# Performance work log

Measured on AMD Instinct MI355X. Metric: run time of the kernel, lower is better.

The kernel has to match this reference:

```python
import jax, jax.numpy as jnp
import numpy as np

B, D, K, NC, F = 2048, 256, 256, 64, 512
EPS = 1e-3           # transport_eps
TAU_MIN = 0.01
TAU_DENOM_MIN = 1e-3


def setup_inputs() -> dict:
    key = jax.random.key(0)
    ks = jax.random.split(key, 8)
    # latents strictly inside the Poincare ball (norm ~0.5 for D=256)
    z = 0.03 * jax.random.normal(ks[0], (B, D), jnp.float32)
    features = jax.random.normal(ks[1], (B, F), jnp.float32)
    # SpectralLinear params (treated as plain linear layers in the reference)
    W_qz = 0.02 * jax.random.normal(ks[2], (K, D), jnp.float32)
    b_qz = jnp.zeros((K,), jnp.float32)
    W_qf = 0.02 * jax.random.normal(ks[3], (K, F), jnp.float32)
    b_qf = jnp.zeros((K,), jnp.float32)
    # full tensorization gamma: [K, D, D]
    q_gamma = 0.02 * jax.random.normal(ks[4], (K, D, D), jnp.float32)
    chart_queries = 0.02 * jax.random.normal(ks[5], (NC, K), jnp.float32)
    return {
        "z": z, "features": features,
        "W_qz": W_qz, "b_qz": b_qz, "W_qf": W_qf, "b_qf": b_qf,
        "q_gamma": q_gamma, "chart_queries": chart_queries,
    }


def reference(z, features, W_qz, b_qz, W_qf, b_qf, q_gamma, chart_queries):
    # centers = chart_queries[:, :latent_dim] (chart_tokens=None path); D == K here
    centers = chart_queries[:, :D]                      # [NC, D]

    # ---- hyperbolic (Poincare ball) distance scores ----
    r2 = jnp.sum(z * z, axis=-1)                        # [B]
    c_sq = jnp.sum(centers * centers, axis=-1)          # [NC]
    diff = z[:, None, :] - centers[None, :, :]          # [B, NC, D]
    dist_sq = jnp.sum(diff * diff, axis=-1)             # [B, NC]
    denom = (1.0 - r2[:, None]) * (1.0 - c_sq[None, :])
    arg = 1.0 + 2.0 * dist_sq / (denom + EPS)
    dist = jnp.arccosh(jnp.maximum(arg, 1.0 + EPS))

    # metric-aware temperature tau(z)
    tau = jnp.maximum(
        jnp.sqrt(jnp.float32(K)) * jnp.maximum(1.0 - r2, TAU_DENOM_MIN) * 0.5,
        TAU_MIN,
    )                                                   # [B]
    scores = -dist / tau[:, None]                       # [B, NC]

    # ---- feature-based refinement (q_feat_proj branch) ----
    q = z @ W_qz.T + b_qz + features @ W_qf.T + b_qf    # [B, K]
    # gamma term: einsum('bij,kij->bk', z outer z, q_gamma) without [B,D,D]
    gz = jnp.einsum('bj,kij->bki', z, q_gamma)          # [B, K, D]
    q = q + jnp.einsum('bki,bi->bk', gz, z)             # [B, K]

    # transported queries: base_queries / lambda(z); (Q/lam) . q == (q @ Q.T)/lam
    r2c = jnp.minimum(r2, 1.0 - EPS)
    lam = 2.0 / (1.0 - r2c + EPS)                       # [B]
    feature_scores = (q @ chart_queries.T) / lam[:, None]  # [B, NC]

    scores = scores + 0.1 * feature_scores / tau[:, None]

    router_weights = jax.nn.softmax(scores, axis=-1)    # [B, NC]
    K_chart = jnp.argmax(router_weights, axis=-1)       # [B]
    return router_weights, K_chart
```

## Files before the change

kernel.cpp:

```cpp
#include <hip/hip_runtime.h>
#include <hip/hip_bf16.h>
#include <hip/hip_fp16.h>


#define B_SZ 2048
#define D_SZ 256
#define K_SZ 256
#define NC_SZ 64
#define F_SZ 512
#define P_SZ 65536

typedef float  floatx4  __attribute__((ext_vector_type(4)));
typedef float  floatx16 __attribute__((ext_vector_type(16)));
typedef _Float16 h8 __attribute__((ext_vector_type(8)));
typedef __fp16  fp16x2 __attribute__((ext_vector_type(2)));
union H8U4 { uint4 u; h8 h; };

#define WS_BEFF  49152
#define WS_CSQ   49216
#define WS_Q2    65664
#define WS_MH    196736
#define WS_WALL  2293888
#define WS_PART  2351232

__device__ __forceinline__ unsigned pkrtz_u(float a, float b) {
    fp16x2 r = __builtin_amdgcn_cvt_pkrtz(a, b);
    return __builtin_bit_cast(unsigned, r);
}
__device__ __forceinline__ _Float16 h16rtz(float x) {
    fp16x2 r = __builtin_amdgcn_cvt_pkrtz(x, x);
    return (_Float16)r[0];
}
__device__ __forceinline__ unsigned packh2(_Float16 a, _Float16 b) {
    union { _Float16 h[2]; unsigned u; } r; r.h[0] = a; r.h[1] = b; return r.u;
}

__device__ __forceinline__ void gload16(const void* g, void* l) {
    __builtin_amdgcn_global_load_lds(
        (const __attribute__((address_space(1))) unsigned*)g,
        (__attribute__((address_space(3))) unsigned*)l, 16, 0, 0);
}

__global__ __launch_bounds__(256) void prep_kernel(
        const float* __restrict__ Wqz, const float* __restrict__ bqz,
        const float* __restrict__ Wqf, const float* __restrict__ bqf,
        const float* __restrict__ cq,  float* __restrict__ ws) {
    const int tid = threadIdx.x;
    const int w = tid >> 6, c = tid & 63;
    const int bid = blockIdx.x;
    char* wall = (char*)(ws + WS_WALL);

    if (bid >= 193) {
        _Float16* cqh = (_Float16*)(ws + WS_Q2);
        const int idx = (bid - 193)*256 + tid;
        const floatx4* sp = (const floatx4*)(cq + idx*8);
        floatx4 a = sp[0], b = sp[1];
        uint4 u = { pkrtz_u(a[0],a[1]), pkrtz_u(a[2],a[3]),
                    pkrtz_u(b[0],b[1]), pkrtz_u(b[2],b[3]) };
        *(uint4*)(cqh + idx*8) = u;
        return;
    }

    __shared__ float cqL[64*257];
    #pragma unroll
    for (int s = 0; s < 16; ++s) {
        const int e4 = s*256 + tid;
        const int row = e4 >> 6, col = (e4 & 63)*4;
        floatx4 v = *(const floatx4*)(cq + e4*4);
        #pragma unroll
        for (int u = 0; u < 4; ++u) cqL[row*257 + col + u] = v[u];
    }
    __syncthreads();

    if (bid < 64) {
        const int i = bid*4 + w;
        float a0 = 0.f, a1 = 0.f, a2 = 0.f, a3 = 0.f;
        #pragma unroll 8
        for (int k = 0; k < K_SZ; k += 4) {
            a0 = fmaf(cqL[c*257 + k    ], Wqz[(k    )*D_SZ + i], a0);
            a1 = fmaf(cqL[c*257 + k + 1], Wqz[(k + 1)*D_SZ + i], a1);
            a2 = fmaf(cqL[c*257 + k + 2], Wqz[(k + 2)*D_SZ + i], a2);
            a3 = fmaf(cqL[c*257 + k + 3], Wqz[(k + 3)*D_SZ + i], a3);
        }
        const float acc = (a0 + a1) + (a2 + a3);
        const int boff = c*512 + ((((i >> 3) & 31) ^ (c & 31)) << 4) + (i & 7)*2;
        *(_Float16*)(wall + 0*32768 + boff) = (_Float16)acc;
        const float v = cqL[c*257 + i];
        const _Float16 vh = (_Float16)v;
        *(_Float16*)(wall + 5*32768 + boff) = vh;
        *(_Float16*)(wall + 6*32768 + boff) =
            h16rtz((v - (float)vh) * 1024.f);
    } else if (bid < 192) {
        const int j = (bid - 64)*4 + w;
        float a0 = 0.f, a1 = 0.f, a2 = 0.f, a3 = 0.f;
        #pragma unroll 8
        for (int k = 0; k < K_SZ; k += 4) {
            a0 = fmaf(cqL[c*257 + k    ], Wqf[(k    )*F_SZ + j], a0);
            a1 = fmaf(cqL[c*257 + k + 1], Wqf[(k + 1)*F_SZ + j], a1);
            a2 = fmaf(cqL[c*257 + k + 2], Wqf[(k + 2)*F_SZ + j], a2);
            a3 = fmaf(cqL[c*257 + k + 3], Wqf[(k + 3)*F_SZ + j], a3);
        }
        const float acc = (a0 + a1) + (a2 + a3);
        const int row = j & 255;
        const int sbase = (j < 256) ? 1 : 3;
        const int boff = c*512 + ((((row >> 3) & 31) ^ (c & 31)) << 4) + (row & 7)*2;
        const _Float16 ah = (_Float16)acc;
        *(_Float16*)(wall + (size_t)sbase*32768 + boff) = ah;
        *(_Float16*)(wall + (size_t)(sbase + 1)*32768 + boff) =
            h16rtz((acc - (float)ah) * 1024.f);
    } else {
        if (w == 0) {
            float acc = 0.f;
            for (int k = 0; k < K_SZ; ++k)
                acc = fmaf(cqL[c*257 + k], bqz[k] + bqf[k], acc);
            ws[WS_BEFF + c] = acc;
        } else if (w == 1) {
            float acc = 0.f;
            for (int i = 0; i < D_SZ; ++i) {
                const float v = cqL[c*257 + i];
                acc = fmaf(v, v, acc);
            }
            ws[WS_CSQ + c] = acc;
        }
    }
}

__global__ __launch_bounds__(256, 4) void mc_kernel(
        const float* __restrict__ gamma, const _Float16* __restrict__ cqh,
        _Float16* __restrict__ mh) {
    const int tid = threadIdx.x;
    const int w = tid >> 6, lane = tid & 63;
    const int ln = lane & 31, half = lane >> 5;
    const int mt = w >> 1, ns = w & 1;
    const int p0 = blockIdx.x * 64;
    const int iseg = p0 >> 8, j0 = p0 & 255;
    const int rot = blockIdx.x & 15;

    floatx16 acc;
    #pragma unroll
    for (int r = 0; r < 16; ++r) acc[r] = 0.f;

    const int arow = mt*32 + ln;
    const float* __restrict__ gbase = gamma + (size_t)(half*8)*P_SZ + p0 + ns*32 + ln;

    #pragma unroll 2
    for (int t = 0; t < 16; ++t) {
        const int kc = (t + rot) & 15;
        float g[8];
        #pragma unroll
        for (int kk = 0; kk < 8; ++kk)
            g[kk] = gbase[(size_t)(kc*16 + kk)*P_SZ];
        H8U4 a; a.u = *(const uint4*)(cqh + arow*256 + kc*16 + half*8);
        H8U4 b;
        b.u.x = pkrtz_u(g[0], g[1]);
        b.u.y = pkrtz_u(g[2], g[3]);
        b.u.z = pkrtz_u(g[4], g[5]);
        b.u.w = pkrtz_u(g[6], g[7]);
        acc = __builtin_amdgcn_mfma_f32_32x32x16_f16(a.h, b.h, acc, 0, 0, 0);
    }
    #pragma unroll
    for (int r = 0; r < 16; ++r) {
        const int cc = mt*32 + (r&3) + 8*(r>>2) + 4*half;
        const int j  = j0 + ns*32 + ln;
        const int jc = j >> 3, off = j & 7;
        mh[(size_t)cc*P_SZ + iseg*256 + ((jc ^ (cc&31))*8 + off)] = (_Float16)acc[r];
    }
}

__global__ __launch_bounds__(256) void qf_kernel(
        const float* __restrict__ z, const _Float16* __restrict__ mh,
        float* __restrict__ part) {
    __shared__ __align__(16) char bt[2][64 * 512];
    const int tid = threadIdx.x;
    const int w = tid >> 6, lane = tid & 63;
    const int ln = lane & 31, half = lane >> 5;
    const int bid = blockIdx.x;
    const int xcd = bid & 7;
    const int y   = bid >> 3;
    const int ig  = xcd*4 + (y & 3);
    const int b0  = (y >> 2) * 128;
    const int bb = b0 + w*32 + ln;

    #define STAGE(i, sel)                                                     \
        _Pragma("unroll")                                                     \
        for (int s = 0; s < 8; ++s) {                                         \
            const int e = s*256 + tid;                                        \
            gload16((const char*)mh +                                         \
                    ((size_t)(e >> 5)*P_SZ + (size_t)(i)*256)*2 + (e & 31)*16,\
                    bt[sel] + e*16);                                          \
        }

    STAGE(ig*8, 0);

    uint4 zjh[16];
    #pragma unroll
    for (int ch = 0; ch < 16; ++ch) {
        const floatx4* zp = (const floatx4*)(z + bb*D_SZ + ch*16 + half*8);
        floatx4 a = zp[0], b = zp[1];
        zjh[ch].x = pkrtz_u(a[0], a[1]);
        zjh[ch].y = pkrtz_u(a[2], a[3]);
        zjh[ch].z = pkrtz_u(b[0], b[1]);
        zjh[ch].w = pkrtz_u(b[2], b[3]);
    }
    float ziv[8];
    {
        const floatx4* zp = (const floatx4*)(z + bb*D_SZ + ig*8);
        floatx4 a = zp[0], b = zp[1];
        #pragma unroll
        for (int t = 0; t < 4; ++t) { ziv[t] = a[t]; ziv[4+t] = b[t]; }
    }

    floatx16 acc0, acc1;
    #pragma unroll
    for (int r = 0; r < 16; ++r) { acc0[r] = 0.f; acc1[r] = 0.f; }

    for (int il = 0; il < 8; ++il) {
        __syncthreads();
        if (il < 7) { STAGE(ig*8 + il + 1, (il + 1) & 1); }

        const float zi = ziv[il];
        const unsigned zu = pkrtz_u(zi, zi);
        H8U4 zb; zb.u.x = zu; zb.u.y = zu; zb.u.z = zu; zb.u.w = zu;
        const char* btc = bt[il & 1];
        __builtin_amdgcn_s_setprio(1);
        #pragma unroll
        for (int ch = 0; ch < 16; ++ch) {
            H8U4 aj; aj.u = zjh[ch];
            h8 af = aj.h * zb.h;
            const int pc = ((ch*2 + half) ^ ln) * 16;
            H8U4 f0, f1;
            f0.u = *(const uint4*)(btc + ln*512 + pc);
            f1.u = *(const uint4*)(btc + (32 + ln)*512 + pc);
            acc0 = __builtin_amdgcn_mfma_f32_32x32x16_f16(af, f0.h, acc0, 0, 0, 0);
            acc1 = __builtin_amdgcn_mfma_f32_32x32x16_f16(af, f1.h, acc1, 0, 0, 0);
        }
        __builtin_amdgcn_s_setprio(0);
    }
    #undef STAGE

    float* __restrict__ qp = part + (size_t)ig * (B_SZ * NC_SZ);
    #pragma unroll
    for (int r = 0; r < 16; ++r) {
        const int row  = (r&3) + 8*(r>>2) + 4*half;
        const int brow = b0 + w*32 + row;
        qp[brow*NC_SZ + ln]      = acc0[r];
        qp[brow*NC_SZ + 32 + ln] = acc1[r];
    }
}

__global__ __launch_bounds__(256) void lin2_kernel(
        const float* __restrict__ z, const float* __restrict__ feat,
        const float* __restrict__ wall_f, float* __restrict__ part,
        float* __restrict__ dot) {
    __shared__ __align__(16) char bt[2][64 * 512];
    const char* wall = (const char*)wall_f;
    const int tid = threadIdx.x;
    const int w = tid >> 6, lane = tid & 63;
    const int ln = lane & 31, half = lane >> 5;
    const int b0 = blockIdx.x * 128;
    const int s  = blockIdx.y;
    const int bb = b0 + w*32 + ln;
    const int s_hi = (s == 0) ? 0 : (s == 1) ? 1 : (s == 2) ? 3 : 5;

    #pragma unroll
    for (int e0 = 0; e0 < 8; ++e0) {
        const int e = e0*256 + tid;
        gload16(wall + s_hi*32768 + e*16, bt[0] + e*16);
    }
    if (s > 0) {
        #pragma unroll
        for (int e0 = 0; e0 < 8; ++e0) {
            const int e = e0*256 + tid;
            gload16(wall + (s_hi + 1)*32768 + e*16, bt[1] + e*16);
        }
    }
    const float* __restrict__ arow =
        (s == 0 || s == 3) ? z + bb*D_SZ : feat + bb*F_SZ + (s == 2 ? 256 : 0);
    __syncthreads();

    floatx16 hh0, hh1, lh0, lh1, hl0, hl1;
    #pragma unroll
    for (int r = 0; r < 16; ++r) {
        hh0[r] = 0.f; hh1[r] = 0.f; lh0[r] = 0.f;
        lh1[r] = 0.f; hl0[r] = 0.f; hl1[r] = 0.f;
    }

    #pragma unroll
    for (int ch = 0; ch < 16; ++ch) {
        const floatx4* ap = (const floatx4*)(arow + ch*16 + half*8);
        floatx4 a4 = ap[0], b4 = ap[1];
        float vv[8];
        #pragma unroll
        for (int t = 0; t < 4; ++t) { vv[t] = a4[t]; vv[4+t] = b4[t]; }
        _Float16 hc[8];
        #pragma unroll
        for (int j = 0; j < 8; ++j) hc[j] = (_Float16)vv[j];
        H8U4 ah;
        ah.u.x = packh2(hc[0], hc[1]); ah.u.y = packh2(hc[2], hc[3]);
        ah.u.z = packh2(hc[4], hc[5]); ah.u.w = packh2(hc[6], hc[7]);

        const int pc = ((ch*2 + half) ^ ln) * 16;
        H8U4 f0, f1;
        f0.u = *(const uint4*)(bt[0] + ln*512 + pc);
        f1.u = *(const uint4*)(bt[0] + (32 + ln)*512 + pc);
        hh0 = __builtin_amdgcn_mfma_f32_32x32x16_f16(ah.h, f0.h, hh0, 0, 0, 0);
        hh1 = __builtin_amdgcn_mfma_f32_32x32x16_f16(ah.h, f1.h, hh1, 0, 0, 0);

        if (s > 0) {
            float l[8];
            #pragma unroll
            for (int j = 0; j < 8; ++j) l[j] = (vv[j] - (float)hc[j]) * 1024.f;
            H8U4 al;
            al.u.x = pkrtz_u(l[0], l[1]); al.u.y = pkrtz_u(l[2], l[3]);
            al.u.z = pkrtz_u(l[4], l[5]); al.u.w = pkrtz_u(l[6], l[7]);
            H8U4 g0, g1;
            g0.u = *(const uint4*)(bt[1] + ln*512 + pc);
            g1.u = *(const uint4*)(bt[1] + (32 + ln)*512 + pc);
            lh0 = __builtin_amdgcn_mfma_f32_32x32x16_f16(al.h, f0.h, lh0, 0, 0, 0);
            lh1 = __builtin_amdgcn_mfma_f32_32x32x16_f16(al.h, f1.h, lh1, 0, 0, 0);
            hl0 = __builtin_amdgcn_mfma_f32_32x32x16_f16(ah.h, g0.h, hl0, 0, 0, 0);
            hl1 = __builtin_amdgcn_mfma_f32_32x32x16_f16(ah.h, g1.h, hl1, 0, 0, 0);
        }
    }

    const float is = 1.0f / 1024.0f;
    float* __restrict__ qp = part + (size_t)(32 + s) * (B_SZ * NC_SZ);
    #pragma unroll
    for (int r = 0; r < 16; ++r) {
        const int row  = (r&3) + 8*(r>>2) + 4*half;
        const int brow = b0 + w*32 + row;
        float v0 = hh0[r], v1 = hh1[r];
        if (s > 0) { v0 += (lh0[r] + hl0[r])*is; v1 += (lh1[r] + hl1[r])*is; }
        if (s < 3) {
            qp[brow*NC_SZ + ln]      = v0;
            qp[brow*NC_SZ + 32 + ln] = v1;
        } else {
            dot[brow*NC_SZ + ln]      = v0;
            dot[brow*NC_SZ + 32 + ln] = v1;
        }
    }
}

__global__ __launch_bounds__(256) void final_kernel(
        const float* __restrict__ z, const float* __restrict__ ws,
        const float* __restrict__ dot, float* __restrict__ out) {
    const int w = threadIdx.x >> 6, c = threadIdx.x & 63;
    const int b = blockIdx.x*4 + w;

    const floatx4 zv = *(const floatx4*)(z + b*D_SZ + c*4);
    float r2 = zv[0]*zv[0] + zv[1]*zv[1] + zv[2]*zv[2] + zv[3]*zv[3];
    #pragma unroll
    for (int off = 32; off > 0; off >>= 1)
        r2 += __shfl_xor(r2, off, 64);

    const float* __restrict__ part = ws + WS_PART;
    float Q = ws[WS_BEFF + c];
    #pragma unroll
    for (int p = 0; p < 35; ++p)
        Q += part[(size_t)p * (B_SZ*NC_SZ) + b*NC_SZ + c];

    const float csq = ws[WS_CSQ + c];
    const float dsq = fmaf(-2.f, dot[b*64 + c], r2) + csq;

    const double r2d = (double)r2, csqd = (double)csq, dsqd = (double)dsq;
    const double denom = (1.0 - r2d) * (1.0 - csqd);
    double arg = 1.0 + 2.0 * dsqd / (denom + 0.001);
    if (arg < 1.001) arg = 1.001;
    const double dist = acosh(arg);
    double tmp = 1.0 - r2d; if (tmp < 0.001) tmp = 0.001;
    double tau = 8.0 * tmp;
    if (tau < 0.01) tau = 0.01;
    double r2c = r2d; if (r2c > 0.999) r2c = 0.999;
    const double lam = 2.0 / (1.0 - r2c + 0.001);
    const double score = -dist / tau + 0.1 * ((double)Q / lam) / tau;

    double m = score;
    #pragma unroll
    for (int off = 32; off > 0; off >>= 1) {
        double o = __shfl_xor(m, off, 64);
        m = fmax(m, o);
    }
    const double e = exp(score - m);
    double s = e;
    #pragma unroll
    for (int off = 32; off > 0; off >>= 1) s += __shfl_xor(s, off, 64);
    out[b*NC_SZ + c] = (float)(e / s);

    double bsc = score; int bix = c;
    #pragma unroll
    for (int off = 32; off > 0; off >>= 1) {
        double osc = __shfl_xor(bsc, off, 64);
        int    oix = __shfl_xor(bix, off, 64);
        if (osc > bsc || (osc == bsc && oix < bix)) { bsc = osc; bix = oix; }
    }
    if (c == 0) out[B_SZ*NC_SZ + b] = (float)bix;
}

extern "C" void kernel_launch(void* const* d_in, const int* in_sizes, int n_in,
                              void* d_out, int out_size, void* d_ws, size_t ws_size,
                              hipStream_t stream) {
    const float* z    = (const float*)d_in[0];
    const float* feat = (const float*)d_in[1];
    const float* Wqz  = (const float*)d_in[2];
    const float* bqz  = (const float*)d_in[3];
    const float* Wqf  = (const float*)d_in[4];
    const float* bqf  = (const float*)d_in[5];
    const float* gamma= (const float*)d_in[6];
    const float* cq   = (const float*)d_in[7];
    float* out = (float*)d_out;
    float* ws  = (float*)d_ws;
    _Float16* cqh = (_Float16*)(ws + WS_Q2);
    _Float16* mh  = (_Float16*)(ws + WS_MH);
    float*    dot = ws + WS_MH;

    prep_kernel<<<201, 256, 0, stream>>>(Wqz, bqz, Wqf, bqf, cq, ws);
    mc_kernel<<<1024, 256, 0, stream>>>(gamma, cqh, mh);
    qf_kernel<<<512, 256, 0, stream>>>(z, mh, ws + WS_PART);
    lin2_kernel<<<dim3(16, 4), 256, 0, stream>>>(z, feat, ws + WS_WALL,
                                                 ws + WS_PART, dot);
    final_kernel<<<512, 256, 0, stream>>>(z, ws, dot, out);
}
```

Measured before the change: 179.2 us.

## Merge prep and gamma-contraction kernels, merge qf and lin2 kernels, halve LDS tiles

Cuts the pipeline from five launches to three. The prep work and the gamma-by-chart-query MFMA contraction now share one grid, with the query-to-fp16 conversion done inline so the separate cqh buffer is gone. The gamma-quadratic partials and the split-fp16 linear projections also run in one grid. LDS tiles are halved (16 KB double buffers, cqL processed in two 128-wide halves) to raise occupancy, at the cost of more stage/sync iterations. The dot output moves to its own workspace region so it no longer aliases mh, which the fused kernel still reads.

```diff
diff --git a/kernel.cpp b/kernel.cpp
--- a/kernel.cpp
+++ b/kernel.cpp
@@ -18,10 +18,10 @@
 
 #define WS_BEFF  49152
 #define WS_CSQ   49216
-#define WS_Q2    65664
 #define WS_MH    196736
 #define WS_WALL  2293888
 #define WS_PART  2351232
+#define WS_DOT   6938752
 
 __device__ __forceinline__ unsigned pkrtz_u(float a, float b) {
     fp16x2 r = __builtin_amdgcn_cvt_pkrtz(a, b);
@@ -41,65 +41,128 @@
         (__attribute__((address_space(3))) unsigned*)l, 16, 0, 0);
 }
 
-__global__ __launch_bounds__(256) void prep_kernel(
-        const float* __restrict__ Wqz, const float* __restrict__ bqz,
-        const float* __restrict__ Wqf, const float* __restrict__ bqf,
-        const float* __restrict__ cq,  float* __restrict__ ws) {
+__global__ __launch_bounds__(256, 4) void mid_kernel(
+        const float* __restrict__ gamma, const float* __restrict__ cq,
+        const float* __restrict__ Wqz,  const float* __restrict__ bqz,
+        const float* __restrict__ Wqf,  const float* __restrict__ bqf,
+        float* __restrict__ ws, _Float16* __restrict__ mh) {
+    __shared__ float cqL[64*129];
     const int tid = threadIdx.x;
+    const int bid = blockIdx.x;
+
+    if (bid < 1024) {
+        const int w = tid >> 6, lane = tid & 63;
+        const int ln = lane & 31, half = lane >> 5;
+        const int mt = w >> 1, ns = w & 1;
+        const int p0 = bid * 64;
+        const int iseg = p0 >> 8, j0 = p0 & 255;
+        const int rot = bid & 15;
+
+        floatx16 acc;
+        #pragma unroll
+        for (int r = 0; r < 16; ++r) acc[r] = 0.f;
+
+        const int arow = mt*32 + ln;
+        const float* __restrict__ cqrow = cq + arow*256;
+        const float* __restrict__ gbase =
+            gamma + (size_t)(half*8)*P_SZ + p0 + ns*32 + ln;
+
+        #pragma unroll 2
+        for (int t = 0; t < 16; ++t) {
+            const int kc = (t + rot) & 15;
+            float g[8];
+            #pragma unroll
+            for (int kk = 0; kk < 8; ++kk)
+                g[kk] = gbase[(size_t)(kc*16 + kk)*P_SZ];
+            const floatx4* cp = (const floatx4*)(cqrow + kc*16 + half*8);
+            floatx4 ca = cp[0], cb = cp[1];
+            H8U4 a;
+            a.u.x = pkrtz_u(ca[0], ca[1]); a.u.y = pkrtz_u(ca[2], ca[3]);
+            a.u.z = pkrtz_u(cb[0], cb[1]); a.u.w = pkrtz_u(cb[2], cb[3]);
+            H8U4 b;
+            b.u.x = pkrtz_u(g[0], g[1]);
+            b.u.y = pkrtz_u(g[2], g[3]);
+            b.u.z = pkrtz_u(g[4], g[5]);
+            b.u.w = pkrtz_u(g[6], g[7]);
+            acc = __builtin_amdgcn_mfma_f32_32x32x16_f16(a.h, b.h, acc, 0, 0, 0);
+        }
+        #pragma unroll
+        for (int r = 0; r < 16; ++r) {
+            const int cc = mt*32 + (r&3) + 8*(r>>2) + 4*half;
+            const int j  = j0 + ns*32 + ln;
+            const int jc = j >> 3, off = j & 7;
+            mh[(size_t)cc*P_SZ + iseg*256 + ((jc ^ (cc&31))*8 + off)] =
+                (_Float16)acc[r];
+        }
+        return;
+    }
+
+    const int pbid = bid - 1024;
     const int w = tid >> 6, c = tid & 63;
-    const int bid = blockIdx.x;
     char* wall = (char*)(ws + WS_WALL);
 
-    if (bid >= 193) {
-        _Float16* cqh = (_Float16*)(ws + WS_Q2);
-        const int idx = (bid - 193)*256 + tid;
-        const floatx4* sp = (const floatx4*)(cq + idx*8);
-        floatx4 a = sp[0], b = sp[1];
-        uint4 u = { pkrtz_u(a[0],a[1]), pkrtz_u(a[2],a[3]),
-                    pkrtz_u(b[0],b[1]), pkrtz_u(b[2],b[3]) };
-        *(uint4*)(cqh + idx*8) = u;
-        return;
-    }
-
-    __shared__ float cqL[64*257];
-    #pragma unroll
-    for (int s = 0; s < 16; ++s) {
-        const int e4 = s*256 + tid;
-        const int row = e4 >> 6, col = (e4 & 63)*4;
-        floatx4 v = *(const floatx4*)(cq + e4*4);
-        #pragma unroll
-        for (int u = 0; u < 4; ++u) cqL[row*257 + col + u] = v[u];
-    }
-    __syncthreads();
-
-    if (bid < 64) {
-        const int i = bid*4 + w;
-        float a0 = 0.f, a1 = 0.f, a2 = 0.f, a3 = 0.f;
-        #pragma unroll 8
-        for (int k = 0; k < K_SZ; k += 4) {
-            a0 = fmaf(cqL[c*257 + k    ], Wqz[(k    )*D_SZ + i], a0);
-            a1 = fmaf(cqL[c*257 + k + 1], Wqz[(k + 1)*D_SZ + i], a1);
-            a2 = fmaf(cqL[c*257 + k + 2], Wqz[(k + 2)*D_SZ + i], a2);
-            a3 = fmaf(cqL[c*257 + k + 3], Wqz[(k + 3)*D_SZ + i], a3);
-        }
-        const float acc = (a0 + a1) + (a2 + a3);
+    float a0 = 0.f, a1 = 0.f, a2 = 0.f, a3 = 0.f;
+    float bacc = 0.f, cacc = 0.f, cqv = 0.f;
+    const int i_or_j = (pbid < 64) ? pbid*4 + w :
+                       (pbid < 192) ? (pbid - 64)*4 + w : 0;
+
+    for (int h = 0; h < 2; ++h) {
+        #pragma unroll
+        for (int s8 = 0; s8 < 8; ++s8) {
+            const int e4 = s8*256 + tid;
+            const int row = e4 >> 5, col4 = (e4 & 31)*4;
+            floatx4 v = *(const floatx4*)(cq + row*256 + h*128 + col4);
+            #pragma unroll
+            for (int u = 0; u < 4; ++u) cqL[row*129 + col4 + u] = v[u];
+        }
+        __syncthreads();
+
+        if (pbid < 64) {
+            const int i = i_or_j;
+            #pragma unroll 8
+            for (int kk = 0; kk < 128; kk += 4) {
+                const int k = h*128 + kk;
+                a0 = fmaf(cqL[c*129 + kk    ], Wqz[(k    )*D_SZ + i], a0);
+                a1 = fmaf(cqL[c*129 + kk + 1], Wqz[(k + 1)*D_SZ + i], a1);
+                a2 = fmaf(cqL[c*129 + kk + 2], Wqz[(k + 2)*D_SZ + i], a2);
+                a3 = fmaf(cqL[c*129 + kk + 3], Wqz[(k + 3)*D_SZ + i], a3);
+            }
+            if ((i >> 7) == h) cqv = cqL[c*129 + (i & 127)];
+        } else if (pbid < 192) {
+            const int j = i_or_j;
+            #pragma unroll 8
+            for (int kk = 0; kk < 128; kk += 4) {
+                const int k = h*128 + kk;
+                a0 = fmaf(cqL[c*129 + kk    ], Wqf[(k    )*F_SZ + j], a0);
+                a1 = fmaf(cqL[c*129 + kk + 1], Wqf[(k + 1)*F_SZ + j], a1);
+                a2 = fmaf(cqL[c*129 + kk + 2], Wqf[(k + 2)*F_SZ + j], a2);
+                a3 = fmaf(cqL[c*129 + kk + 3], Wqf[(k + 3)*F_SZ + j], a3);
+            }
+        } else {
+            if (w == 0) {
+                for (int kk = 0; kk < 128; ++kk) {
+                    const int k = h*128 + kk;
+                    bacc = fmaf(cqL[c*129 + kk], bqz[k] + bqf[k], bacc);
+                }
+            } else if (w == 1) {
+                for (int ii = 0; ii < 128; ++ii) {
+                    const float v = cqL[c*129 + ii];
+                    cacc = fmaf(v, v, cacc);
+                }
+            }
+        }
+        __syncthreads();
+    }
+
+    if (pbid < 64) {
+        const int i = i_or_j;
         const int boff = c*512 + ((((i >> 3) & 31) ^ (c & 31)) << 4) + (i & 7)*2;
-        *(_Float16*)(wall + 0*32768 + boff) = (_Float16)acc;
-        const float v = cqL[c*257 + i];
-        const _Float16 vh = (_Float16)v;
+        *(_Float16*)(wall + 0*32768 + boff) = (_Float16)((a0 + a1) + (a2 + a3));
+        const _Float16 vh = (_Float16)cqv;
         *(_Float16*)(wall + 5*32768 + boff) = vh;
-        *(_Float16*)(wall + 6*32768 + boff) =
-            h16rtz((v - (float)vh) * 1024.f);
-    } else if (bid < 192) {
-        const int j = (bid - 64)*4 + w;
-        float a0 = 0.f, a1 = 0.f, a2 = 0.f, a3 = 0.f;
-        #pragma unroll 8
-        for (int k = 0; k < K_SZ; k += 4) {
-            a0 = fmaf(cqL[c*257 + k    ], Wqf[(k    )*F_SZ + j], a0);
-            a1 = fmaf(cqL[c*257 + k + 1], Wqf[(k + 1)*F_SZ + j], a1);
-            a2 = fmaf(cqL[c*257 + k + 2], Wqf[(k + 2)*F_SZ + j], a2);
-            a3 = fmaf(cqL[c*257 + k + 3], Wqf[(k + 3)*F_SZ + j], a3);
-        }
+        *(_Float16*)(wall + 6*32768 + boff) = h16rtz((cqv - (float)vh) * 1024.f);
+    } else if (pbid < 192) {
+        const int j = i_or_j;
         const float acc = (a0 + a1) + (a2 + a3);
         const int row = j & 255;
         const int sbase = (j < 256) ? 1 : 3;
@@ -109,174 +172,119 @@
         *(_Float16*)(wall + (size_t)(sbase + 1)*32768 + boff) =
             h16rtz((acc - (float)ah) * 1024.f);
     } else {
-        if (w == 0) {
-            float acc = 0.f;
-            for (int k = 0; k < K_SZ; ++k)
-                acc = fmaf(cqL[c*257 + k], bqz[k] + bqf[k], acc);
-            ws[WS_BEFF + c] = acc;
-        } else if (w == 1) {
-            float acc = 0.f;
-            for (int i = 0; i < D_SZ; ++i) {
-                const float v = cqL[c*257 + i];
-                acc = fmaf(v, v, acc);
-            }
-            ws[WS_CSQ + c] = acc;
-        }
-    }
-}
-
-__global__ __launch_bounds__(256, 4) void mc_kernel(
-        const float* __restrict__ gamma, const _Float16* __restrict__ cqh,
-        _Float16* __restrict__ mh) {
+        if (w == 0) ws[WS_BEFF + c] = bacc;
+        else if (w == 1) ws[WS_CSQ + c] = cacc;
+    }
+}
+
+__global__ __launch_bounds__(256, 3) void qflin_kernel(
+        const float* __restrict__ z, const float* __restrict__ feat,
+        const _Float16* __restrict__ mh, const float* __restrict__ wall_f,
+        float* __restrict__ part, float* __restrict__ dot) {
+    __shared__ __align__(16) char bt[2][16384];
     const int tid = threadIdx.x;
     const int w = tid >> 6, lane = tid & 63;
     const int ln = lane & 31, half = lane >> 5;
-    const int mt = w >> 1, ns = w & 1;
-    const int p0 = blockIdx.x * 64;
-    const int iseg = p0 >> 8, j0 = p0 & 255;
-    const int rot = blockIdx.x & 15;
-
-    floatx16 acc;
-    #pragma unroll
-    for (int r = 0; r < 16; ++r) acc[r] = 0.f;
-
-    const int arow = mt*32 + ln;
-    const float* __restrict__ gbase = gamma + (size_t)(half*8)*P_SZ + p0 + ns*32 + ln;
-
-    #pragma unroll 2
-    for (int t = 0; t < 16; ++t) {
-        const int kc = (t + rot) & 15;
-        float g[8];
-        #pragma unroll
-        for (int kk = 0; kk < 8; ++kk)
-            g[kk] = gbase[(size_t)(kc*16 + kk)*P_SZ];
-        H8U4 a; a.u = *(const uint4*)(cqh + arow*256 + kc*16 + half*8);
-        H8U4 b;
-        b.u.x = pkrtz_u(g[0], g[1]);
-        b.u.y = pkrtz_u(g[2], g[3]);
-        b.u.z = pkrtz_u(g[4], g[5]);
-        b.u.w = pkrtz_u(g[6], g[7]);
-        acc = __builtin_amdgcn_mfma_f32_32x32x16_f16(a.h, b.h, acc, 0, 0, 0);
-    }
-    #pragma unroll
-    for (int r = 0; r < 16; ++r) {
-        const int cc = mt*32 + (r&3) + 8*(r>>2) + 4*half;
-        const int j  = j0 + ns*32 + ln;
-        const int jc = j >> 3, off = j & 7;
-        mh[(size_t)cc*P_SZ + iseg*256 + ((jc ^ (cc&31))*8 + off)] = (_Float16)acc[r];
-    }
-}
-
-__global__ __launch_bounds__(256) void qf_kernel(
-        const float* __restrict__ z, const _Float16* __restrict__ mh,
-        float* __restrict__ part) {
-    __shared__ __align__(16) char bt[2][64 * 512];
-    const int tid = threadIdx.x;
-    const int w = tid >> 6, lane = tid & 63;
-    const int ln = lane & 31, half = lane >> 5;
-    const int bid = blockIdx.x;
-    const int xcd = bid & 7;
-    const int y   = bid >> 3;
-    const int ig  = xcd*4 + (y & 3);
-    const int b0  = (y >> 2) * 128;
-    const int bb = b0 + w*32 + ln;
-
-    #define STAGE(i, sel)                                                     \
-        _Pragma("unroll")                                                     \
-        for (int s = 0; s < 8; ++s) {                                         \
-            const int e = s*256 + tid;                                        \
-            gload16((const char*)mh +                                         \
-                    ((size_t)(e >> 5)*P_SZ + (size_t)(i)*256)*2 + (e & 31)*16,\
-                    bt[sel] + e*16);                                          \
-        }
-
-    STAGE(ig*8, 0);
-
-    uint4 zjh[16];
-    #pragma unroll
-    for (int ch = 0; ch < 16; ++ch) {
-        const floatx4* zp = (const floatx4*)(z + bb*D_SZ + ch*16 + half*8);
-        floatx4 a = zp[0], b = zp[1];
-        zjh[ch].x = pkrtz_u(a[0], a[1]);
-        zjh[ch].y = pkrtz_u(a[2], a[3]);
-        zjh[ch].z = pkrtz_u(b[0], b[1]);
-        zjh[ch].w = pkrtz_u(b[2], b[3]);
-    }
-    float ziv[8];
-    {
-        const floatx4* zp = (const floatx4*)(z + bb*D_SZ + ig*8);
-        floatx4 a = zp[0], b = zp[1];
-        #pragma unroll
-        for (int t = 0; t < 4; ++t) { ziv[t] = a[t]; ziv[4+t] = b[t]; }
-    }
-
-    floatx16 acc0, acc1;
-    #pragma unroll
-    for (int r = 0; r < 16; ++r) { acc0[r] = 0.f; acc1[r] = 0.f; }
-
-    for (int il = 0; il < 8; ++il) {
-        __syncthreads();
-        if (il < 7) { STAGE(ig*8 + il + 1, (il + 1) & 1); }
-
-        const float zi = ziv[il];
-        const unsigned zu = pkrtz_u(zi, zi);
-        H8U4 zb; zb.u.x = zu; zb.u.y = zu; zb.u.z = zu; zb.u.w = zu;
-        const char* btc = bt[il & 1];
-        __builtin_amdgcn_s_setprio(1);
+
+    if (blockIdx.x >= 64) {
+        const int bid = blockIdx.x - 64;
+        const int xcd = bid & 7;
+        const int y   = bid >> 3;
+        const int ig  = xcd*4 + (y & 3);
+        const int b0  = (y >> 2) * 128;
+        const int bb  = b0 + w*32 + ln;
+
+        #define STAGE_Q(ii, hs, sel)                                          \
+            _Pragma("unroll")                                                 \
+            for (int e0 = 0; e0 < 4; ++e0) {                                  \
+                const int e = e0*256 + tid;                                   \
+                const int cc = e >> 4, up = e & 15;                           \
+                const int u = (((hs) ^ ((cc >> 4) & 1)) << 4) | up;           \
+                gload16((const char*)mh +                                     \
+                        ((size_t)cc*P_SZ + (size_t)(ii)*256)*2 + u*16,        \
+                        bt[sel] + e*16);                                      \
+            }
+
+        STAGE_Q(ig*8, 0, 0);
+
+        uint4 zjh[16];
         #pragma unroll
         for (int ch = 0; ch < 16; ++ch) {
-            H8U4 aj; aj.u = zjh[ch];
-            h8 af = aj.h * zb.h;
-            const int pc = ((ch*2 + half) ^ ln) * 16;
-            H8U4 f0, f1;
-            f0.u = *(const uint4*)(btc + ln*512 + pc);
-            f1.u = *(const uint4*)(btc + (32 + ln)*512 + pc);
-            acc0 = __builtin_amdgcn_mfma_f32_32x32x16_f16(af, f0.h, acc0, 0, 0, 0);
-            acc1 = __builtin_amdgcn_mfma_f32_32x32x16_f16(af, f1.h, acc1, 0, 0, 0);
-        }
-        __builtin_amdgcn_s_setprio(0);
-    }
-    #undef STAGE
-
-    float* __restrict__ qp = part + (size_t)ig * (B_SZ * NC_SZ);
-    #pragma unroll
-    for (int r = 0; r < 16; ++r) {
-        const int row  = (r&3) + 8*(r>>2) + 4*half;
-        const int brow = b0 + w*32 + row;
-        qp[brow*NC_SZ + ln]      = acc0[r];
-        qp[brow*NC_SZ + 32 + ln] = acc1[r];
-    }
-}
-
-__global__ __launch_bounds__(256) void lin2_kernel(
-        const float* __restrict__ z, const float* __restrict__ feat,
-        const float* __restrict__ wall_f, float* __restrict__ part,
-        float* __restrict__ dot) {
-    __shared__ __align__(16) char bt[2][64 * 512];
+            const floatx4* zp = (const floatx4*)(z + bb*D_SZ + ch*16 + half*8);
+            floatx4 a = zp[0], b = zp[1];
+            zjh[ch].x = pkrtz_u(a[0], a[1]);
+            zjh[ch].y = pkrtz_u(a[2], a[3]);
+            zjh[ch].z = pkrtz_u(b[0], b[1]);
+            zjh[ch].w = pkrtz_u(b[2], b[3]);
+        }
+        float ziv[8];
+        {
+            const floatx4* zp = (const floatx4*)(z + bb*D_SZ + ig*8);
+            floatx4 a = zp[0], b = zp[1];
+            #pragma unroll
+            for (int t = 0; t < 4; ++t) { ziv[t] = a[t]; ziv[4+t] = b[t]; }
+        }
+
+        floatx16 acc0, acc1;
+        #pragma unroll
+        for (int r = 0; r < 16; ++r) { acc0[r] = 0.f; acc1[r] = 0.f; }
+
+        for (int t = 0; t < 16; ++t) {
+            __syncthreads();
+            if (t < 15) {
+                const int tn = t + 1;
+                STAGE_Q(ig*8 + (tn >> 1), tn & 1, tn & 1);
+            }
+            const int il = t >> 1, hs = t & 1;
+            const float zi = ziv[il];
+            const unsigned zu = pkrtz_u(zi, zi);
+            H8U4 zb; zb.u.x = zu; zb.u.y = zu; zb.u.z = zu; zb.u.w = zu;
+            const char* btc = bt[t & 1];
+            __builtin_amdgcn_s_setprio(1);
+            #pragma unroll
+            for (int chp = 0; chp < 8; ++chp) {
+                H8U4 aj; aj.u = zjh[hs*8 + chp];
+                h8 af = aj.h * zb.h;
+                const int po = (((chp*2 + half) ^ (ln & 15)) << 4);
+                H8U4 f0, f1;
+                f0.u = *(const uint4*)(btc + ln*256 + po);
+                f1.u = *(const uint4*)(btc + 8192 + ln*256 + po);
+                acc0 = __builtin_amdgcn_mfma_f32_32x32x16_f16(af, f0.h, acc0, 0, 0, 0);
+                acc1 = __builtin_amdgcn_mfma_f32_32x32x16_f16(af, f1.h, acc1, 0, 0, 0);
+            }
+            __builtin_amdgcn_s_setprio(0);
+        }
+        #undef STAGE_Q
+
+        float* __restrict__ qp = part + (size_t)ig * (B_SZ * NC_SZ);
+        #pragma unroll
+        for (int r = 0; r < 16; ++r) {
+            const int row  = (r&3) + 8*(r>>2) + 4*half;
+            const int brow = b0 + w*32 + row;
+            qp[brow*NC_SZ + ln]      = acc0[r];
+            qp[brow*NC_SZ + 32 + ln] = acc1[r];
+        }
+        return;
+    }
+
     const char* wall = (const char*)wall_f;
-    const int tid = threadIdx.x;
-    const int w = tid >> 6, lane = tid & 63;
-    const int ln = lane & 31, half = lane >> 5;
-    const int b0 = blockIdx.x * 128;
-    const int s  = blockIdx.y;
+    const int lbid = blockIdx.x;
+    const int b0 = (lbid >> 2) * 128;
+    const int s  = lbid & 3;
     const int bb = b0 + w*32 + ln;
     const int s_hi = (s == 0) ? 0 : (s == 1) ? 1 : (s == 2) ? 3 : 5;
-
-    #pragma unroll
-    for (int e0 = 0; e0 < 8; ++e0) {
-        const int e = e0*256 + tid;
-        gload16(wall + s_hi*32768 + e*16, bt[0] + e*16);
-    }
-    if (s > 0) {
-        #pragma unroll
-        for (int e0 = 0; e0 < 8; ++e0) {
-            const int e = e0*256 + tid;
-            gload16(wall + (s_hi + 1)*32768 + e*16, bt[1] + e*16);
-        }
-    }
     const float* __restrict__ arow =
         (s == 0 || s == 3) ? z + bb*D_SZ : feat + bb*F_SZ + (s == 2 ? 256 : 0);
-    __syncthreads();
+
+    #define STAGE_L(img, h, sel)                                              \
+        _Pragma("unroll")                                                     \
+        for (int e0 = 0; e0 < 4; ++e0) {                                      \
+            const int e = e0*256 + tid;                                       \
+            const int cc = e >> 4, up = e & 15;                               \
+            const int u = (((h) ^ ((cc >> 4) & 1)) << 4) | up;                \
+            gload16(wall + (size_t)(img)*32768 + cc*512 + u*16,               \
+                    bt[sel] + e*16);                                          \
+        }
 
     floatx16 hh0, hh1, lh0, lh1, hl0, hl1;
     #pragma unroll
@@ -285,43 +293,52 @@
         lh1[r] = 0.f; hl0[r] = 0.f; hl1[r] = 0.f;
     }
 
-    #pragma unroll
-    for (int ch = 0; ch < 16; ++ch) {
-        const floatx4* ap = (const floatx4*)(arow + ch*16 + half*8);
-        floatx4 a4 = ap[0], b4 = ap[1];
-        float vv[8];
-        #pragma unroll
-        for (int t = 0; t < 4; ++t) { vv[t] = a4[t]; vv[4+t] = b4[t]; }
-        _Float16 hc[8];
-        #pragma unroll
-        for (int j = 0; j < 8; ++j) hc[j] = (_Float16)vv[j];
-        H8U4 ah;
-        ah.u.x = packh2(hc[0], hc[1]); ah.u.y = packh2(hc[2], hc[3]);
-        ah.u.z = packh2(hc[4], hc[5]); ah.u.w = packh2(hc[6], hc[7]);
-
-        const int pc = ((ch*2 + half) ^ ln) * 16;
-        H8U4 f0, f1;
-        f0.u = *(const uint4*)(bt[0] + ln*512 + pc);
-        f1.u = *(const uint4*)(bt[0] + (32 + ln)*512 + pc);
-        hh0 = __builtin_amdgcn_mfma_f32_32x32x16_f16(ah.h, f0.h, hh0, 0, 0, 0);
-        hh1 = __builtin_amdgcn_mfma_f32_32x32x16_f16(ah.h, f1.h, hh1, 0, 0, 0);
-
-        if (s > 0) {
-            float l[8];
-            #pragma unroll
-            for (int j = 0; j < 8; ++j) l[j] = (vv[j] - (float)hc[j]) * 1024.f;
-            H8U4 al;
-            al.u.x = pkrtz_u(l[0], l[1]); al.u.y = pkrtz_u(l[2], l[3]);
-            al.u.z = pkrtz_u(l[4], l[5]); al.u.w = pkrtz_u(l[6], l[7]);
-            H8U4 g0, g1;
-            g0.u = *(const uint4*)(bt[1] + ln*512 + pc);
-            g1.u = *(const uint4*)(bt[1] + (32 + ln)*512 + pc);
-            lh0 = __builtin_amdgcn_mfma_f32_32x32x16_f16(al.h, f0.h, lh0, 0, 0, 0);
-            lh1 = __builtin_amdgcn_mfma_f32_32x32x16_f16(al.h, f1.h, lh1, 0, 0, 0);
-            hl0 = __builtin_amdgcn_mfma_f32_32x32x16_f16(ah.h, g0.h, hl0, 0, 0, 0);
-            hl1 = __builtin_amdgcn_mfma_f32_32x32x16_f16(ah.h, g1.h, hl1, 0, 0, 0);
-        }
-    }
+    for (int h = 0; h < 2; ++h) {
+        STAGE_L(s_hi, h, 0);
+        if (s > 0) { STAGE_L(s_hi + 1, h, 1); }
+        __syncthreads();
+
+        #pragma unroll
+        for (int chp = 0; chp < 8; ++chp) {
+            const int kb = h*128 + chp*16 + half*8;
+            const floatx4* ap = (const floatx4*)(arow + kb);
+            floatx4 a4 = ap[0], b4 = ap[1];
+            float vv[8];
+            #pragma unroll
+            for (int t = 0; t < 4; ++t) { vv[t] = a4[t]; vv[4+t] = b4[t]; }
+            _Float16 hc[8];
+            #pragma unroll
+            for (int j = 0; j < 8; ++j) hc[j] = (_Float16)vv[j];
+            H8U4 ah;
+            ah.u.x = packh2(hc[0], hc[1]); ah.u.y = packh2(hc[2], hc[3]);
+            ah.u.z = packh2(hc[4], hc[5]); ah.u.w = packh2(hc[6], hc[7]);
+
+            const int po = (((chp*2 + half) ^ (ln & 15)) << 4);
+            H8U4 f0, f1;
+            f0.u = *(const uint4*)(bt[0] + ln*256 + po);
+            f1.u = *(const uint4*)(bt[0] + 8192 + ln*256 + po);
+            hh0 = __builtin_amdgcn_mfma_f32_32x32x16_f16(ah.h, f0.h, hh0, 0, 0, 0);
+            hh1 = __builtin_amdgcn_mfma_f32_32x32x16_f16(ah.h, f1.h, hh1, 0, 0, 0);
+
+            if (s > 0) {
+                float l[8];
+                #pragma unroll
+                for (int j = 0; j < 8; ++j) l[j] = (vv[j] - (float)hc[j]) * 1024.f;
+                H8U4 al;
+                al.u.x = pkrtz_u(l[0], l[1]); al.u.y = pkrtz_u(l[2], l[3]);
+                al.u.z = pkrtz_u(l[4], l[5]); al.u.w = pkrtz_u(l[6], l[7]);
+                H8U4 g0, g1;
+                g0.u = *(const uint4*)(bt[1] + ln*256 + po);
+                g1.u = *(const uint4*)(bt[1] + 8192 + ln*256 + po);
+                lh0 = __builtin_amdgcn_mfma_f32_32x32x16_f16(al.h, f0.h, lh0, 0, 0, 0);
+                lh1 = __builtin_amdgcn_mfma_f32_32x32x16_f16(al.h, f1.h, lh1, 0, 0, 0);
+                hl0 = __builtin_amdgcn_mfma_f32_32x32x16_f16(ah.h, g0.h, hl0, 0, 0, 0);
+                hl1 = __builtin_amdgcn_mfma_f32_32x32x16_f16(ah.h, g1.h, hl1, 0, 0, 0);
+            }
+        }
+        if (h == 0) __syncthreads();
+    }
+    #undef STAGE_L
 
     const float is = 1.0f / 1024.0f;
     float* __restrict__ qp = part + (size_t)(32 + s) * (B_SZ * NC_SZ);
@@ -409,14 +426,10 @@
     const float* cq   = (const float*)d_in[7];
     float* out = (float*)d_out;
     float* ws  = (float*)d_ws;
-    _Float16* cqh = (_Float16*)(ws + WS_Q2);
-    _Float16* mh  = (_Float16*)(ws + WS_MH);
-    float*    dot = ws + WS_MH;
-
-    prep_kernel<<<201, 256, 0, stream>>>(Wqz, bqz, Wqf, bqf, cq, ws);
-    mc_kernel<<<1024, 256, 0, stream>>>(gamma, cqh, mh);
-    qf_kernel<<<512, 256, 0, stream>>>(z, mh, ws + WS_PART);
-    lin2_kernel<<<dim3(16, 4), 256, 0, stream>>>(z, feat, ws + WS_WALL,
-                                                 ws + WS_PART, dot);
-    final_kernel<<<512, 256, 0, stream>>>(z, ws, dot, out);
-}
+    _Float16* mh = (_Float16*)(ws + WS_MH);
+
+    mid_kernel<<<1217, 256, 0, stream>>>(gamma, cq, Wqz, bqz, Wqf, bqf, ws, mh);
+    qflin_kernel<<<576, 256, 0, stream>>>(z, feat, mh, ws + WS_WALL,
+                                          ws + WS_PART, ws + WS_DOT);
+    final_kernel<<<512, 256, 0, stream>>>(z, ws, ws + WS_DOT, out);
+}
```

Result: faster. 166.0 us (-7.4%).
